# Kernel optimization log

Measured on AMD Instinct MI355X. Metric: run time of the kernel, lower is better.

The kernel has to match this reference:

```python
import jax, jax.numpy as jnp
import numpy as np

D_MODEL = 1024
N_HEADS = 16
HEAD_DIM = D_MODEL // N_HEADS  # 64
SEQ = 2048
BATCH = 1
LOG2_E = 1.44269504


def _rope_freqs(seq, head_dim, theta=10000.0):
    inv_freq = 1.0 / (theta ** (np.arange(0, head_dim, 2, dtype=np.float32) / head_dim))
    angles = np.outer(np.arange(seq, dtype=np.float32), inv_freq)  # [seq, head_dim/2]
    return jnp.asarray(np.cos(angles)), jnp.asarray(np.sin(angles))


def setup_inputs() -> dict:
    key = jax.random.key(0)
    ks = jax.random.split(key, 5)
    scale = 1.0 / np.sqrt(D_MODEL)
    x = jax.random.normal(ks[0], (BATCH, SEQ, D_MODEL), dtype=jnp.float32)
    wq = jax.random.normal(ks[1], (D_MODEL, D_MODEL), dtype=jnp.float32) * scale
    wk = jax.random.normal(ks[2], (D_MODEL, D_MODEL), dtype=jnp.float32) * scale
    wv = jax.random.normal(ks[3], (D_MODEL, D_MODEL), dtype=jnp.float32) * scale
    wo = jax.random.normal(ks[4], (D_MODEL, D_MODEL), dtype=jnp.float32) * scale
    freqs_cos, freqs_sin = _rope_freqs(SEQ, HEAD_DIM)
    return {"x": x, "wq": wq, "wk": wk, "wv": wv, "wo": wo,
            "freqs_cos": freqs_cos, "freqs_sin": freqs_sin}


def _apply_rope(x, cos, sin):
    # x: [b, s, h, d]; cos/sin: [s, d/2]. Complex multiply on (even, odd) pairs.
    xr = x.reshape(x.shape[:-1] + (HEAD_DIM // 2, 2))
    x0, x1 = xr[..., 0], xr[..., 1]
    c = cos[None, :, None, :]
    s = sin[None, :, None, :]
    o0 = x0 * c - x1 * s
    o1 = x0 * s + x1 * c
    return jnp.stack([o0, o1], axis=-1).reshape(x.shape)


def reference(x, wq, wk, wv, wo, freqs_cos, freqs_sin):
    b, s, _ = x.shape
    # Linear(bias=False): y = x @ W.T (torch convention)
    q = (x @ wq.T).reshape(b, s, N_HEADS, HEAD_DIM)
    k = (x @ wk.T).reshape(b, s, N_HEADS, HEAD_DIM)
    v = (x @ wv.T).reshape(b, s, N_HEADS, HEAD_DIM)
    q = _apply_rope(q, freqs_cos, freqs_sin)
    k = _apply_rope(k, freqs_cos, freqs_sin)
    # -> [b, h, s, d]
    q = q.transpose(0, 2, 1, 3)
    k = k.transpose(0, 2, 1, 3)
    v = v.transpose(0, 2, 1, 3)
    scores = jnp.einsum('bhqd,bhkd->bhqk', q, k) * (HEAD_DIM ** -0.5)
    log_w = jax.nn.log_softmax(scores, axis=-1)
    attn_weights = jnp.exp(log_w)
    entropy = (-jnp.sum(attn_weights * log_w, axis=-1) * LOG2_E).transpose(0, 2, 1)  # [b, s, h]
    out = jnp.einsum('bhqk,bhkd->bhqd', attn_weights, v)
    out = out.transpose(0, 2, 1, 3).reshape(b, s, -1)
    return out @ wo.T, attn_weights, entropy
```

## Files before the change

### kernel.cpp

```cpp
#include <hip/hip_runtime.h>
#include <hip/hip_bf16.h>


typedef __attribute__((ext_vector_type(8))) unsigned short u16x8;
typedef __attribute__((ext_vector_type(8))) short s16x8;
typedef __attribute__((ext_vector_type(4))) float f32x4;

__device__ __forceinline__ unsigned short f2b(float f) {
  unsigned int u = __float_as_uint(f);
  return (unsigned short)((u + 0x7fffu + ((u >> 16) & 1u)) >> 16);
}

__device__ __forceinline__ unsigned int f2b2(float a, float b) {
  __hip_bfloat162 h = __float22bfloat162_rn(make_float2(a, b));
  union { __hip_bfloat162 h; unsigned int u; } cv; cv.h = h; return cv.u;
}

__device__ __forceinline__ float b2f(unsigned short u) {
  union { unsigned int u; float f; } cv; cv.u = ((unsigned int)u) << 16; return cv.f;
}

__device__ __forceinline__ int swz64(int row, int col)  { return row * 64  + (col ^ ((row & 7) << 3)); }
__device__ __forceinline__ int swz128(int row, int col) { return row * 128 + (col ^ ((row & 7) << 3)); }

__device__ __forceinline__ void gload16(const void* g, void* l) {
  __builtin_amdgcn_global_load_lds((const __attribute__((address_space(1))) void*)g,
                                   (__attribute__((address_space(3))) void*)l, 16, 0, 0);
}

__global__ __launch_bounds__(256) void cast_all_kernel(const float* __restrict__ x,
    const float* __restrict__ wq, const float* __restrict__ wk, const float* __restrict__ wv,
    const float* __restrict__ wo, unsigned short* __restrict__ xbf,
    unsigned short* __restrict__ wbf, unsigned short* __restrict__ wobf) {
  int i = blockIdx.x * 256 + threadIdx.x;
  const float* src;
  unsigned short* dst;
  if (i < 262144) {
    src = x + (size_t)i * 8; dst = xbf + (size_t)i * 8;
  } else {
    int j = i - 262144;
    int seg = j >> 17, rem = j & 131071;
    if (seg == 3)      { src = wo + (size_t)rem * 8; dst = wobf + (size_t)rem * 8; }
    else if (seg == 0) { src = wq + (size_t)rem * 8; dst = wbf + (size_t)rem * 8; }
    else if (seg == 1) { src = wk + (size_t)rem * 8; dst = wbf + 1048576 + (size_t)rem * 8; }
    else               { src = wv + (size_t)rem * 8; dst = wbf + 2097152 + (size_t)rem * 8; }
  }
  u16x8 o;
#pragma unroll
  for (int j = 0; j < 8; ++j) o[j] = f2b(src[j]);
  *(u16x8*)dst = o;
}

__global__ __launch_bounds__(256) void gemm_qkv_kernel(const unsigned short* __restrict__ A,
    const unsigned short* __restrict__ B, const float* __restrict__ fcos,
    const float* __restrict__ fsin, unsigned short* __restrict__ qbf,
    unsigned short* __restrict__ kbf, unsigned short* __restrict__ vt) {
  const int K = 1024;
  int bx = blockIdx.x;
  int m0 = blockIdx.y * 128;
  int n0 = bx * 128;
  int tid = threadIdx.x, lane = tid & 63, w = tid >> 6;
  int cl = lane & 15, hw = lane >> 4;
  int wr = (w >> 1) * 64, wc = (w & 1) * 64;
  int l8 = lane >> 3, o8 = lane & 7;

  __shared__ unsigned short smem[32768];
  unsigned short* As = smem;
  unsigned short* Bs = smem + 16384;

  const unsigned short* gA = A + (size_t)(m0 + w * 8 + l8) * K + (o8 ^ l8) * 8;
  const unsigned short* gB = B + (size_t)(n0 + w * 8 + l8) * K + (o8 ^ l8) * 8;

  auto stage = [&](int buf, int k0) {
    unsigned short* as = As + buf * 8192;
    unsigned short* bs = Bs + buf * 8192;
#pragma unroll
    for (int j = 0; j < 4; ++j) {
      gload16(gA + (size_t)(32 * j) * K + k0, as + j * 2048 + w * 512);
      gload16(gB + (size_t)(32 * j) * K + k0, bs + j * 2048 + w * 512);
    }
  };

  f32x4 acc[4][4];
#pragma unroll
  for (int i = 0; i < 4; ++i)
#pragma unroll
    for (int j = 0; j < 4; ++j) acc[i][j] = (f32x4){0.f, 0.f, 0.f, 0.f};

  stage(0, 0);
  __syncthreads();
  for (int t = 0; t < 16; ++t) {
    if (t < 15) stage((t + 1) & 1, (t + 1) * 64);
    const unsigned short* as = As + (t & 1) * 8192;
    const unsigned short* bs = Bs + (t & 1) * 8192;
#pragma unroll
    for (int kk = 0; kk < 2; ++kk) {
      s16x8 af[4], bf[4];
#pragma unroll
      for (int i = 0; i < 4; ++i)
        af[i] = *(const s16x8*)(as + swz64(wr + i * 16 + cl, kk * 32 + hw * 8));
#pragma unroll
      for (int j = 0; j < 4; ++j)
        bf[j] = *(const s16x8*)(bs + swz64(wc + j * 16 + cl, kk * 32 + hw * 8));
#pragma unroll
      for (int i = 0; i < 4; ++i)
#pragma unroll
        for (int j = 0; j < 4; ++j)
          acc[i][j] = __builtin_amdgcn_mfma_f32_16x16x32_bf16(af[i], bf[j], acc[i][j], 0, 0, 0);
    }
    __syncthreads();
  }

  int sel = bx >> 3;
  if (sel < 2) {
    float tscl = (sel == 0) ? 0.18033688f : 1.0f;
    float* cosl = (float*)smem;
    float* sinl = cosl + 128 * 33;
    for (int t = tid; t < 4096; t += 256) {
      cosl[(t >> 5) * 33 + (t & 31)] = fcos[(size_t)m0 * 32 + t] * tscl;
      sinl[(t >> 5) * 33 + (t & 31)] = fsin[(size_t)m0 * 32 + t] * tscl;
    }
    __syncthreads();
    unsigned short* dst = sel ? kbf : qbf;
    int cbase = (bx & 7) * 128;
#pragma unroll
    for (int i = 0; i < 4; ++i)
#pragma unroll
      for (int j = 0; j < 4; ++j)
#pragma unroll
        for (int r = 0; r < 4; ++r) {
          int rl = wr + i * 16 + hw * 4 + r;
          int c = cbase + wc + j * 16 + cl;
          float v = acc[i][j][r];
          float pvv = __shfl_xor(v, 1);
          int pair = (c & 63) >> 1;
          float cc = cosl[rl * 33 + pair];
          float ss = sinl[rl * 33 + pair];
          float o = (c & 1) ? (pvv * ss + v * cc) : (v * cc - pvv * ss);
          dst[(size_t)(m0 + rl) * 1024 + c] = f2b(o);
        }
  } else {
    unsigned short* T = smem;
#pragma unroll
    for (int i = 0; i < 4; ++i)
#pragma unroll
      for (int j = 0; j < 4; ++j) {
        int dl = wc + j * 16 + cl;
        int sl = wr + i * 16 + hw * 4;
        ushort4 pk;
        pk.x = f2b(acc[i][j][0]); pk.y = f2b(acc[i][j][1]);
        pk.z = f2b(acc[i][j][2]); pk.w = f2b(acc[i][j][3]);
        *(ushort4*)(T + swz128(dl, sl)) = pk;
      }
    __syncthreads();
    int dbase = (bx & 7) * 128;
    for (int t = tid; t < 2048; t += 256) {
      int dl = t >> 4, sl = (t & 15) << 3;
      u16x8 val = *(const u16x8*)(T + swz128(dl, sl));
      *(u16x8*)(vt + (size_t)(dbase + dl) * 2048 + m0 + sl) = val;
    }
  }
}

__global__ __launch_bounds__(256) void gemm_out_kernel(const unsigned short* __restrict__ A,
    const unsigned short* __restrict__ B, float* __restrict__ C) {
  const int K = 1024, N = 1024;
  int n0 = blockIdx.x * 64, m0 = blockIdx.y * 128;
  int tid = threadIdx.x, lane = tid & 63, w = tid >> 6;
  int cl = lane & 15, hw = lane >> 4;
  int wr = w * 32;
  int l8 = lane >> 3, o8 = lane & 7;

  __shared__ unsigned short As[2 * 8192], Bs[2 * 4096];

  int loct = o8 ^ l8;
  const unsigned short* gA = A + (size_t)(m0 + wr + l8) * K + loct * 8;
  const unsigned short* gB = B + (size_t)(n0 + w * 16 + l8) * K + loct * 8;

  auto stage = [&](int buf, int k0) {
    unsigned short* as = As + buf * 8192;
    unsigned short* bs = Bs + buf * 4096;
#pragma unroll
    for (int j = 0; j < 4; ++j)
      gload16(gA + (size_t)(8 * j) * K + k0, as + (wr + 8 * j) * 64);
#pragma unroll
    for (int j = 0; j < 2; ++j)
      gload16(gB + (size_t)(8 * j) * K + k0, bs + (w * 16 + 8 * j) * 64);
  };

  f32x4 acc[2][4];
#pragma unroll
  for (int i = 0; i < 2; ++i)
#pragma unroll
    for (int j = 0; j < 4; ++j) acc[i][j] = (f32x4){0.f, 0.f, 0.f, 0.f};

  stage(0, 0);
  __syncthreads();
  for (int t = 0; t < 16; ++t) {
    if (t < 15) stage((t + 1) & 1, (t + 1) * 64);
    const unsigned short* as = As + (t & 1) * 8192;
    const unsigned short* bs = Bs + (t & 1) * 4096;
#pragma unroll
    for (int kk = 0; kk < 2; ++kk) {
      s16x8 af[2], bf[4];
#pragma unroll
      for (int i = 0; i < 2; ++i)
        af[i] = *(const s16x8*)(as + swz64(wr + i * 16 + cl, kk * 32 + hw * 8));
#pragma unroll
      for (int j = 0; j < 4; ++j)
        bf[j] = *(const s16x8*)(bs + swz64(j * 16 + cl, kk * 32 + hw * 8));
#pragma unroll
      for (int i = 0; i < 2; ++i)
#pragma unroll
        for (int j = 0; j < 4; ++j)
          acc[i][j] = __builtin_amdgcn_mfma_f32_16x16x32_bf16(af[i], bf[j], acc[i][j], 0, 0, 0);
    }
    __syncthreads();
  }
#pragma unroll
  for (int i = 0; i < 2; ++i)
#pragma unroll
    for (int j = 0; j < 4; ++j)
#pragma unroll
      for (int r = 0; r < 4; ++r)
        C[(size_t)(m0 + wr + i * 16 + hw * 4 + r) * N + n0 + j * 16 + cl] = acc[i][j][r];
}

__global__ __launch_bounds__(256, 4) void attn_kernel(const unsigned short* __restrict__ Qbf,
                                                      const unsigned short* __restrict__ Kbf,
                                                      const unsigned short* __restrict__ Vt,
                                                      float* __restrict__ attnw,
                                                      float* __restrict__ ent,
                                                      unsigned short* __restrict__ attno) {
  int h = blockIdx.x, qb = blockIdx.y;
  int q0 = qb * 64;
  int tid = threadIdx.x, lane = tid & 63, w = tid >> 6;
  int qr = w * 16, cl = lane & 15, hw = lane >> 4;
  int l8 = lane >> 3, o8 = lane & 7;

  __shared__ unsigned short smem[20480];
  unsigned short* Ps = smem;

  const unsigned short* gK = Kbf + h * 64 + (o8 ^ l8) * 8;
  const unsigned short* gV = Vt + (size_t)(h * 64) * 2048 + (o8 ^ l8) * 8;

  auto stageK128 = [&](int b, int kc) {
    unsigned short* dst = smem + 4096 + b * 8192 + w * 2048;
#pragma unroll
    for (int i = 0; i < 4; ++i)
      gload16(gK + (size_t)(kc + w * 32 + i * 8 + l8) * 1024, dst + i * 512);
  };
  auto stageK64 = [&](int b, int kc) {
    unsigned short* dst = smem + 4096 + b * 4096 + w * 1024;
#pragma unroll
    for (int i = 0; i < 2; ++i)
      gload16(gK + (size_t)(kc + w * 16 + i * 8 + l8) * 1024, dst + i * 512);
  };
  auto stageV64 = [&](int b, int kc) {
    unsigned short* dst = smem + 12288 + b * 4096 + w * 1024;
#pragma unroll
    for (int i = 0; i < 2; ++i)
      gload16(gV + (size_t)(w * 16 + i * 8 + l8) * 2048 + kc, dst + i * 512);
  };

  const unsigned short* qrow = Qbf + (size_t)(q0 + qr + cl) * 1024 + h * 64 + hw * 8;
  s16x8 qa0 = *(const s16x8*)(qrow);
  s16x8 qa1 = *(const s16x8*)(qrow + 32);

  float l_acc = 0.f, es_acc = 0.f;

  stageK128(0, 0);
  __syncthreads();
  for (int t = 0; t < 16; ++t) {
    if (t < 15) stageK128((t + 1) & 1, (t + 1) * 128);
    const unsigned short* ks = smem + 4096 + (t & 1) * 8192;
#pragma unroll
    for (int j = 0; j < 8; ++j) {
      f32x4 c = (f32x4){0.f, 0.f, 0.f, 0.f};
      s16x8 kf0 = *(const s16x8*)(ks + swz64(j * 16 + cl, hw * 8));
      s16x8 kf1 = *(const s16x8*)(ks + swz64(j * 16 + cl, 32 + hw * 8));
      c = __builtin_amdgcn_mfma_f32_16x16x32_bf16(kf0, qa0, c, 0, 0, 0);
      c = __builtin_amdgcn_mfma_f32_16x16x32_bf16(kf1, qa1, c, 0, 0, 0);
#pragma unroll
      for (int r = 0; r < 4; ++r) {
        float e = __builtin_amdgcn_exp2f(c[r]);
        l_acc += e;
        es_acc = fmaf(e, c[r], es_acc);
      }
    }
    __syncthreads();
  }

  stageK64(0, 0);
  stageV64(0, 0);

  l_acc += __shfl_xor(l_acc, 16);  l_acc += __shfl_xor(l_acc, 32);
  es_acc += __shfl_xor(es_acc, 16); es_acc += __shfl_xor(es_acc, 32);
  float log2l = __builtin_amdgcn_logf(l_acc);
  float bias = -log2l;
  if (lane < 16)
    ent[(size_t)(q0 + qr + lane) * 16 + h] = log2l - es_acc / l_acc;

  f32x4 pv[4];
#pragma unroll
  for (int dj = 0; dj < 4; ++dj) pv[dj] = (f32x4){0.f, 0.f, 0.f, 0.f};

  float* awbase = attnw + ((size_t)h << 22) + (size_t)q0 * 2048;

  __syncthreads();
  for (int t = 0; t < 32; ++t) {
    if (t < 31) { stageK64((t + 1) & 1, (t + 1) * 64); stageV64((t + 1) & 1, (t + 1) * 64); }
    int kc = t * 64;
    const unsigned short* ks = smem + 4096 + (t & 1) * 4096;
    const unsigned short* vs = smem + 12288 + (t & 1) * 4096;
#pragma unroll
    for (int j = 0; j < 4; ++j) {
      f32x4 c = (f32x4){0.f, 0.f, 0.f, 0.f};
      s16x8 kf0 = *(const s16x8*)(ks + swz64(j * 16 + cl, hw * 8));
      s16x8 kf1 = *(const s16x8*)(ks + swz64(j * 16 + cl, 32 + hw * 8));
      c = __builtin_amdgcn_mfma_f32_16x16x32_bf16(kf0, qa0, c, 0, 0, 0);
      c = __builtin_amdgcn_mfma_f32_16x16x32_bf16(kf1, qa1, c, 0, 0, 0);
      f32x4 p;
#pragma unroll
      for (int r = 0; r < 4; ++r) p[r] = __builtin_amdgcn_exp2f(c[r] + bias);
      uint2 pk;
      pk.x = f2b2(p[0], p[1]);
      pk.y = f2b2(p[2], p[3]);
      *(uint2*)(Ps + swz64(qr + cl, j * 16 + hw * 4)) = pk;
    }
    s16x8 pa[2];
#pragma unroll
    for (int kk2 = 0; kk2 < 2; ++kk2)
      pa[kk2] = *(const s16x8*)(Ps + swz64(qr + cl, kk2 * 32 + hw * 8));
#pragma unroll
    for (int dj = 0; dj < 4; ++dj) {
      f32x4 cc = pv[dj];
#pragma unroll
      for (int kk2 = 0; kk2 < 2; ++kk2) {
        s16x8 vb = *(const s16x8*)(vs + swz64(dj * 16 + cl, kk2 * 32 + hw * 8));
        cc = __builtin_amdgcn_mfma_f32_16x16x32_bf16(pa[kk2], vb, cc, 0, 0, 0);
      }
      pv[dj] = cc;
    }
    int kq = cl * 4;
#pragma unroll
    for (int i = 0; i < 4; ++i) {
      int row = qr + i * 4 + hw;
      ushort4 pb = *(const ushort4*)(Ps + swz64(row, kq));
      f32x4 pf;
      pf[0] = b2f(pb.x); pf[1] = b2f(pb.y); pf[2] = b2f(pb.z); pf[3] = b2f(pb.w);
      *(f32x4*)(awbase + (size_t)row * 2048 + kc + kq) = pf;
    }
    __syncthreads();
  }

#pragma unroll
  for (int dj = 0; dj < 4; ++dj)
#pragma unroll
    for (int r = 0; r < 4; ++r) {
      int row = q0 + qr + hw * 4 + r;
      int col = h * 64 + dj * 16 + cl;
      attno[(size_t)row * 1024 + col] = f2b(pv[dj][r]);
    }
}

extern "C" void kernel_launch(void* const* d_in, const int* in_sizes, int n_in,
                              void* d_out, int out_size, void* d_ws, size_t ws_size,
                              hipStream_t stream) {
  const float* x  = (const float*)d_in[0];
  const float* wq = (const float*)d_in[1];
  const float* wk = (const float*)d_in[2];
  const float* wv = (const float*)d_in[3];
  const float* wo = (const float*)d_in[4];
  const float* fc = (const float*)d_in[5];
  const float* fs = (const float*)d_in[6];

  float* out0  = (float*)d_out;
  float* attnw = out0 + (size_t)2048 * 1024;
  float* ent   = attnw + (size_t)16 * 2048 * 2048;

  char* ws = (char*)d_ws;
  unsigned short* xbf  = (unsigned short*)(ws);
  unsigned short* wbf  = (unsigned short*)(ws + (4u  << 20));
  unsigned short* wobf = (unsigned short*)(ws + (10u << 20));
  unsigned short* qbf  = (unsigned short*)(ws + (12u << 20));
  unsigned short* kbf  = (unsigned short*)(ws + (16u << 20));
  unsigned short* vtbf = (unsigned short*)(ws + (20u << 20));
  unsigned short* aobf = (unsigned short*)(ws + (24u << 20));

  cast_all_kernel<<<3072, 256, 0, stream>>>(x, wq, wk, wv, wo, xbf, wbf, wobf);
  gemm_qkv_kernel<<<dim3(24, 16), 256, 0, stream>>>(xbf, wbf, fc, fs, qbf, kbf, vtbf);
  attn_kernel<<<dim3(16, 32), 256, 0, stream>>>(qbf, kbf, vtbf, attnw, ent, aobf);
  gemm_out_kernel<<<dim3(16, 16), 256, 0, stream>>>(aobf, wobf, out0);
}
```

Baseline: 125.1 us.

## Split attention key range across two wave groups per block with reduction

Doubles the attention block to 512 threads. Two groups of four waves each cover half of the key sequence for the same 64 query rows. Softmax statistics are combined through shared memory, and the PV partial sums from the second group are added into the first before the output is written. This halves the serial key loop per wave and raises the wave count per block. The cost is double the LDS per block (80KB), which may cut the number of resident blocks, plus extra barriers.

Measured after the change: 124.8 us. No clear change (-0.3%).

```diff
diff --git a/kernel.cpp b/kernel.cpp
--- a/kernel.cpp
+++ b/kernel.cpp
@@ -226,7 +226,7 @@
         C[(size_t)(m0 + wr + i * 16 + hw * 4 + r) * N + n0 + j * 16 + cl] = acc[i][j][r];
 }
 
-__global__ __launch_bounds__(256, 4) void attn_kernel(const unsigned short* __restrict__ Qbf,
+__global__ __launch_bounds__(512, 4) void attn_kernel(const unsigned short* __restrict__ Qbf,
                                                       const unsigned short* __restrict__ Kbf,
                                                       const unsigned short* __restrict__ Vt,
                                                       float* __restrict__ attnw,
@@ -235,32 +235,34 @@
   int h = blockIdx.x, qb = blockIdx.y;
   int q0 = qb * 64;
   int tid = threadIdx.x, lane = tid & 63, w = tid >> 6;
-  int qr = w * 16, cl = lane & 15, hw = lane >> 4;
+  int wh = w & 3, h2 = w >> 2;
+  int qr = wh * 16, cl = lane & 15, hw = lane >> 4;
   int l8 = lane >> 3, o8 = lane & 7;
-
-  __shared__ unsigned short smem[20480];
-  unsigned short* Ps = smem;
+  int kbase = h2 * 1024;
+
+  __shared__ unsigned short smem[40960];
+  unsigned short* Ps = smem + h2 * 4096;
 
   const unsigned short* gK = Kbf + h * 64 + (o8 ^ l8) * 8;
   const unsigned short* gV = Vt + (size_t)(h * 64) * 2048 + (o8 ^ l8) * 8;
 
   auto stageK128 = [&](int b, int kc) {
-    unsigned short* dst = smem + 4096 + b * 8192 + w * 2048;
+    unsigned short* dst = smem + 8192 + h2 * 16384 + b * 8192 + (wh * 32) * 64;
 #pragma unroll
     for (int i = 0; i < 4; ++i)
-      gload16(gK + (size_t)(kc + w * 32 + i * 8 + l8) * 1024, dst + i * 512);
+      gload16(gK + (size_t)(kc + wh * 32 + i * 8 + l8) * 1024, dst + i * 512);
   };
   auto stageK64 = [&](int b, int kc) {
-    unsigned short* dst = smem + 4096 + b * 4096 + w * 1024;
+    unsigned short* dst = smem + 8192 + h2 * 8192 + b * 4096 + (wh * 16) * 64;
 #pragma unroll
     for (int i = 0; i < 2; ++i)
-      gload16(gK + (size_t)(kc + w * 16 + i * 8 + l8) * 1024, dst + i * 512);
+      gload16(gK + (size_t)(kc + wh * 16 + i * 8 + l8) * 1024, dst + i * 512);
   };
   auto stageV64 = [&](int b, int kc) {
-    unsigned short* dst = smem + 12288 + b * 4096 + w * 1024;
+    unsigned short* dst = smem + 24576 + h2 * 8192 + b * 4096 + (wh * 16) * 64;
 #pragma unroll
     for (int i = 0; i < 2; ++i)
-      gload16(gV + (size_t)(w * 16 + i * 8 + l8) * 2048 + kc, dst + i * 512);
+      gload16(gV + (size_t)(wh * 16 + i * 8 + l8) * 2048 + kc, dst + i * 512);
   };
 
   const unsigned short* qrow = Qbf + (size_t)(q0 + qr + cl) * 1024 + h * 64 + hw * 8;
@@ -269,11 +271,11 @@
 
   float l_acc = 0.f, es_acc = 0.f;
 
-  stageK128(0, 0);
-  __syncthreads();
-  for (int t = 0; t < 16; ++t) {
-    if (t < 15) stageK128((t + 1) & 1, (t + 1) * 128);
-    const unsigned short* ks = smem + 4096 + (t & 1) * 8192;
+  stageK128(0, kbase);
+  __syncthreads();
+  for (int t = 0; t < 8; ++t) {
+    if (t < 7) stageK128((t + 1) & 1, kbase + (t + 1) * 128);
+    const unsigned short* ks = smem + 8192 + h2 * 16384 + (t & 1) * 8192;
 #pragma unroll
     for (int j = 0; j < 8; ++j) {
       f32x4 c = (f32x4){0.f, 0.f, 0.f, 0.f};
@@ -291,14 +293,22 @@
     __syncthreads();
   }
 
-  stageK64(0, 0);
-  stageV64(0, 0);
+  stageK64(0, kbase);
+  stageV64(0, kbase);
 
   l_acc += __shfl_xor(l_acc, 16);  l_acc += __shfl_xor(l_acc, 32);
   es_acc += __shfl_xor(es_acc, 16); es_acc += __shfl_xor(es_acc, 32);
+  float* red = (float*)smem;
+  if (lane < 16) { red[(w * 16 + lane) * 2] = l_acc; red[(w * 16 + lane) * 2 + 1] = es_acc; }
+  __syncthreads();
+  {
+    int pr = ((w ^ 4) * 16 + cl) * 2;
+    l_acc += red[pr];
+    es_acc += red[pr + 1];
+  }
   float log2l = __builtin_amdgcn_logf(l_acc);
   float bias = -log2l;
-  if (lane < 16)
+  if (w < 4 && lane < 16)
     ent[(size_t)(q0 + qr + lane) * 16 + h] = log2l - es_acc / l_acc;
 
   f32x4 pv[4];
@@ -308,11 +318,12 @@
   float* awbase = attnw + ((size_t)h << 22) + (size_t)q0 * 2048;
 
   __syncthreads();
-  for (int t = 0; t < 32; ++t) {
-    if (t < 31) { stageK64((t + 1) & 1, (t + 1) * 64); stageV64((t + 1) & 1, (t + 1) * 64); }
-    int kc = t * 64;
-    const unsigned short* ks = smem + 4096 + (t & 1) * 4096;
-    const unsigned short* vs = smem + 12288 + (t & 1) * 4096;
+
+  for (int t = 0; t < 16; ++t) {
+    if (t < 15) { stageK64((t + 1) & 1, kbase + (t + 1) * 64); stageV64((t + 1) & 1, kbase + (t + 1) * 64); }
+    int kc = kbase + t * 64;
+    const unsigned short* ks = smem + 8192 + h2 * 8192 + (t & 1) * 4096;
+    const unsigned short* vs = smem + 24576 + h2 * 8192 + (t & 1) * 4096;
 #pragma unroll
     for (int j = 0; j < 4; ++j) {
       f32x4 c = (f32x4){0.f, 0.f, 0.f, 0.f};
@@ -354,14 +365,26 @@
     __syncthreads();
   }
 
-#pragma unroll
-  for (int dj = 0; dj < 4; ++dj)
-#pragma unroll
-    for (int r = 0; r < 4; ++r) {
-      int row = q0 + qr + hw * 4 + r;
-      int col = h * 64 + dj * 16 + cl;
-      attno[(size_t)row * 1024 + col] = f2b(pv[dj][r]);
-    }
+  float* pvb = (float*)(smem + 8192);
+  if (h2 == 1) {
+#pragma unroll
+    for (int dj = 0; dj < 4; ++dj)
+      *(f32x4*)(pvb + (dj * 256 + wh * 64 + lane) * 4) = pv[dj];
+  }
+  __syncthreads();
+  if (h2 == 0) {
+#pragma unroll
+    for (int dj = 0; dj < 4; ++dj) {
+      f32x4 o = *(const f32x4*)(pvb + (dj * 256 + wh * 64 + lane) * 4);
+      pv[dj] += o;
+#pragma unroll
+      for (int r = 0; r < 4; ++r) {
+        int row = q0 + qr + hw * 4 + r;
+        int col = h * 64 + dj * 16 + cl;
+        attno[(size_t)row * 1024 + col] = f2b(pv[dj][r]);
+      }
+    }
+  }
 }
 
 extern "C" void kernel_launch(void* const* d_in, const int* in_sizes, int n_in,
@@ -390,6 +413,6 @@
 
   cast_all_kernel<<<3072, 256, 0, stream>>>(x, wq, wk, wv, wo, xbf, wbf, wobf);
   gemm_qkv_kernel<<<dim3(24, 16), 256, 0, stream>>>(xbf, wbf, fc, fs, qbf, kbf, vtbf);
-  attn_kernel<<<dim3(16, 32), 256, 0, stream>>>(qbf, kbf, vtbf, attnw, ent, aobf);
+  attn_kernel<<<dim3(16, 32), 512, 0, stream>>>(qbf, kbf, vtbf, attnw, ent, aobf);
   gemm_out_kernel<<<dim3(16, 16), 256, 0, stream>>>(aobf, wobf, out0);
 }
```
